# Optimization experiments

Hardware: AMD Instinct MI355X
Metric: run time of the kernel (lower is better)

Reference implementation:

```python
import jax, jax.numpy as jnp
import numpy as np

B = 4096          # batch_size
D_EMB = 16        # per-side embedding dim (embed_to_from width = 2*D_EMB)
D_HIGH = 784      # flattened high-dim feature size
NSR = 5           # negative_sample_rate
A = 1.576943      # UMAP _a
B_PARAM = 0.8950608  # UMAP _b
REPULSION = 1.0
EPS = 1e-4
GLOBAL_LOSS = 0.5
TOTAL_STEPS = 1000
BATCH_COUNT = 500  # fixed step for deterministic alpha/beta
WARMUP = int(0.05 * TOTAL_STEPS)


def _safe_sqrt(sq):
    # sqrt with zero (not NaN) gradient at 0, matching zero-distance pairs
    safe = jnp.where(sq > 0, sq, 1.0)
    return jnp.where(sq > 0, jnp.sqrt(safe), 0.0)


def _pairwise_dist(x):
    # ||x_i - x_j|| via gram trick; avoids materializing [N,N,D]
    sq = jnp.sum(x * x, axis=1)                      # [N]
    gram = x @ x.T                                   # [N,N]
    d2 = sq[:, None] + sq[None, :] - 2.0 * gram
    return _safe_sqrt(jnp.maximum(d2, 0.0))


def _umap_ce_loss(embed_to_from, perm):
    e_to, e_from = jnp.split(embed_to_from, 2, axis=1)   # [B, D_EMB] each
    neg_to = jnp.repeat(e_to, NSR, axis=0)               # [B*NSR, D_EMB]
    repeat_neg = jnp.repeat(e_from, NSR, axis=0)
    neg_from = repeat_neg[perm]                          # shuffled negatives
    d_pos = _safe_sqrt(jnp.sum((e_to - e_from) ** 2, axis=1))
    d_neg = _safe_sqrt(jnp.sum((neg_to - neg_from) ** 2, axis=1))
    dist = jnp.concatenate([d_pos, d_neg], axis=0)       # [B*(1+NSR)]
    p_dist = 1.0 / (1.0 + A * dist ** (2.0 * B_PARAM))
    p_graph = jnp.concatenate([jnp.ones(B, p_dist.dtype), jnp.zeros(B * NSR, p_dist.dtype)])
    attraction = -p_graph * jnp.log(jnp.clip(p_dist, EPS, 1.0))
    repellant = -(1.0 - p_graph) * jnp.log(jnp.clip(1.0 - p_dist, EPS, 1.0)) * REPULSION
    return jnp.mean(attraction + repellant)


def _global_feature_loss(embed_to_from, to_x):
    e_to = embed_to_from[:, :D_EMB]
    to_x = to_x.reshape(to_x.shape[0], -1)
    high_dis = _pairwise_dist(to_x)     # [N,N]
    low_dis = _pairwise_dist(e_to)      # [N,N]
    # row-wise pearson correlation between high_dis and low_dis
    h = high_dis - jnp.mean(high_dis, axis=1, keepdims=True)
    l = low_dis - jnp.mean(low_dis, axis=1, keepdims=True)
    num = jnp.sum(h * l, axis=1)
    den = jnp.sqrt(jnp.sum(h * h, axis=1)) * jnp.sqrt(jnp.sum(l * l, axis=1))
    corr = jnp.mean(num / den)
    return -corr


def _alpha_beta():
    if BATCH_COUNT >= WARMUP:
        if BATCH_COUNT <= 0.9 * TOTAL_STEPS:
            beta = max(0.0, GLOBAL_LOSS * (1 - BATCH_COUNT / (TOTAL_STEPS - WARMUP * 4)) ** 2)
        else:
            beta = 0.0
        alpha = max(0.0, 1 - beta)
    else:
        alpha = 0.0
        beta = GLOBAL_LOSS
    return alpha, beta


def setup_inputs() -> dict:
    key = jax.random.key(0)
    k1, k2, k3 = jax.random.split(key, 3)
    embed_to_from = jax.random.normal(k1, (B, 2 * D_EMB), dtype=jnp.float32)
    placeholder = jax.random.normal(k2, (B, D_HIGH), dtype=jnp.float32)
    perm = jax.random.permutation(k3, B * NSR).astype(jnp.int32)
    return {"embed_to_from": embed_to_from, "placeholder": placeholder, "perm": perm}


def reference(embed_to_from, placeholder, perm):
    loss = _umap_ce_loss(embed_to_from, perm)
    loss_g = _global_feature_loss(embed_to_from, placeholder)
    alpha, beta = _alpha_beta()
    return alpha * loss + beta * loss_g
```

## Files before the change

kernel.cpp:

```cpp
#include <hip/hip_runtime.h>
#include <hip/hip_bf16.h>
#include <math.h>

#define NB    4096
#define DH    784
#define KX8   832
#define NSR   5
#define NNEG  (NB*NSR)
#define NTOT  (NB + NNEG)

#define A_CONST 1.576943f
#define PEXP    1.7901216f
#define EPS_C   1.0e-4f
#define ALPHA_C 0.9296875f
#define BETA_C  0.0703125f

#define NSLOT 64
#define SLAB  (NB * NSLOT)
#define NBLK  528
#define BUFB  8192

typedef __hip_bfloat16 bf16;
typedef short bf16x8 __attribute__((ext_vector_type(8)));
typedef float f32x4  __attribute__((ext_vector_type(4)));
typedef long long2v __attribute__((ext_vector_type(2)));

#define WS_XF8    0
#define WS_EBF    3407872
#define WS_SQX    3670016
#define WS_SQE    3686400
#define WS_STATSP 3702784
#define WS_UPART  8945664
#define WS_CPART  8946048
#define WS_CNT    8946304

__device__ __forceinline__ void gl2lds16(const void* g, void* l) {
    __builtin_amdgcn_global_load_lds(
        (const __attribute__((address_space(1))) unsigned int*)g,
        (__attribute__((address_space(3))) unsigned int*)l,
        16, 0, 0);
}

__global__ void prep_fused(const float* __restrict__ X, const float* __restrict__ emb,
                           const int* __restrict__ perm, unsigned char* __restrict__ Xf8,
                           float* __restrict__ sqx, bf16* __restrict__ Ebf,
                           float* __restrict__ sqe, float* __restrict__ upart,
                           unsigned* __restrict__ cnt) {
    if (blockIdx.x == 0 && threadIdx.x == 0) *cnt = 0u;
    if (blockIdx.x < 1024) {
        const int wave = threadIdx.x >> 6, lane = threadIdx.x & 63;
        const int row = blockIdx.x * 4 + wave;
        const float4* xr = (const float4*)(X + (size_t)row * DH);
        int* xb = (int*)(Xf8 + (size_t)row * KX8);
        float s = 0.f;
        #pragma unroll
        for (int it = 0; it < 4; ++it) {
            const int idx = lane + it * 64;
            if (idx < 208) {
                const int c = idx >> 4, p = idx & 15;
                const int q = p >> 2, h = (p >> 1) & 1, w = p & 1;
                const int src = c * 16 + h * 8 + q * 2 + w;
                int pk = 0;
                if (src < 196) {
                    float4 v = xr[src];
                    s += v.x * v.x + v.y * v.y + v.z * v.z + v.w * v.w;
                    int lo = __builtin_amdgcn_cvt_pk_fp8_f32(v.x, v.y, 0, false);
                    pk = __builtin_amdgcn_cvt_pk_fp8_f32(v.z, v.w, lo, true);
                }
                xb[idx] = pk;
            }
        }
        #pragma unroll
        for (int off = 32; off; off >>= 1) s += __shfl_down(s, off, 64);
        if (lane == 0) sqx[row] = s;
        return;
    }
    const int ub = blockIdx.x - 1024;
    const int t = ub * 256 + threadIdx.x;
    float val = 0.f;
    if (t < NB) {
        const float4* av = (const float4*)(emb + (size_t)t * 32);
        float4 t0 = av[0], t1 = av[1], t2 = av[2], t3 = av[3];
        float4 f0 = av[4], f1 = av[5], f2 = av[6], f3 = av[7];
        bf16* eb = Ebf + (size_t)t * 32;
        union { bf16 h[4]; ushort4 u; } cv;
        #define ST4(dst, q) cv.h[0]=__float2bfloat16(q.x); cv.h[1]=__float2bfloat16(q.y); \
                            cv.h[2]=__float2bfloat16(q.z); cv.h[3]=__float2bfloat16(q.w); \
                            *(ushort4*)(dst) = cv.u;
        ST4(eb,      t0) ST4(eb + 4,  t1) ST4(eb + 8,  t2) ST4(eb + 12, t3)
        #undef ST4
        ushort4 z = {0, 0, 0, 0};
        *(ushort4*)(eb + 16) = z; *(ushort4*)(eb + 20) = z;
        *(ushort4*)(eb + 24) = z; *(ushort4*)(eb + 28) = z;
        sqe[t] = t0.x*t0.x + t0.y*t0.y + t0.z*t0.z + t0.w*t0.w
               + t1.x*t1.x + t1.y*t1.y + t1.z*t1.z + t1.w*t1.w
               + t2.x*t2.x + t2.y*t2.y + t2.z*t2.z + t2.w*t2.w
               + t3.x*t3.x + t3.y*t3.y + t3.z*t3.z + t3.w*t3.w;
        float d2 = 0.f;
        #define D2(a, b) { float4 df = {a.x-b.x, a.y-b.y, a.z-b.z, a.w-b.w}; \
                           d2 += df.x*df.x + df.y*df.y + df.z*df.z + df.w*df.w; }
        D2(t0, f0) D2(t1, f1) D2(t2, f2) D2(t3, f3)
        #undef D2
        float d = sqrtf(d2);
        float p = 1.f / (1.f + A_CONST * powf(d, PEXP));
        val = -logf(fminf(fmaxf(p, EPS_C), 1.f));
    } else if (t < NTOT) {
        const int k = t - NB;
        const int ti = k / 5;
        const int fi = perm[k] / 5;
        const float4* at = (const float4*)(emb + (size_t)ti * 32);
        const float4* bt = (const float4*)(emb + (size_t)fi * 32 + 16);
        float d2 = 0.f;
        #pragma unroll
        for (int q = 0; q < 4; ++q) {
            float4 a = at[q], b = bt[q];
            float4 df = {a.x-b.x, a.y-b.y, a.z-b.z, a.w-b.w};
            d2 += df.x*df.x + df.y*df.y + df.z*df.z + df.w*df.w;
        }
        float d = sqrtf(d2);
        float p = 1.f / (1.f + A_CONST * powf(d, PEXP));
        val = -logf(fminf(fmaxf(1.f - p, EPS_C), 1.f));
    }
    #pragma unroll
    for (int off = 32; off; off >>= 1) val += __shfl_down(val, off, 64);
    __shared__ float ps[4];
    if ((threadIdx.x & 63) == 0) ps[threadIdx.x >> 6] = val;
    __syncthreads();
    if (threadIdx.x == 0) upart[ub] = ps[0] + ps[1] + ps[2] + ps[3];
}

__global__ __launch_bounds__(256, 3) void gram_kernel(
    const unsigned char* __restrict__ Xf8, const bf16* __restrict__ Ebf,
    const float* __restrict__ sqx, const float* __restrict__ sqe,
    float* __restrict__ statsp) {
    __shared__ unsigned char As[3 * BUFB];
    __shared__ unsigned char Bs[3 * BUFB];
    __shared__ float sqxs[256];
    __shared__ float sqes[256];

    int n = (blockIdx.x & 7) * 66 + (blockIdx.x >> 3);
    int bi = 0;
    while (n >= 32 - bi) { n -= 32 - bi; ++bi; }
    const int bj = bi + n;
    const int i0 = bi * 128, j0 = bj * 128;

    const int tid  = threadIdx.x;
    const int wave = tid >> 6;
    const int lane = tid & 63;
    const int wy = wave >> 1, wx = wave & 1;
    const int quad = lane >> 4, l15 = lane & 15;

    f32x4 acc[4][4];
    #pragma unroll
    for (int a = 0; a < 4; ++a)
        #pragma unroll
        for (int b = 0; b < 4; ++b)
            acc[a][b] = (f32x4){0.f, 0.f, 0.f, 0.f};

    const int c0  = wave * 2;
    const int rA  = lane >> 2;
    const int gsb = (((lane & 3) ^ ((lane >> 3) & 3))) * 16;

    const unsigned char* gA0 = Xf8 + (size_t)(i0 + c0 * 16 + rA) * KX8 + gsb;
    const unsigned char* gA1 = Xf8 + (size_t)(i0 + c0 * 16 + 16 + rA) * KX8 + gsb;
    const unsigned char* gB0 = Xf8 + (size_t)(j0 + c0 * 16 + rA) * KX8 + gsb;
    const unsigned char* gB1 = Xf8 + (size_t)(j0 + c0 * 16 + 16 + rA) * KX8 + gsb;

    if (tid < 128) {
        sqxs[tid] = sqx[i0 + tid]; sqxs[128 + tid] = sqx[j0 + tid];
        sqes[tid] = sqe[i0 + tid]; sqes[128 + tid] = sqe[j0 + tid];
    }
    __syncthreads();

    #pragma unroll
    for (int s = 0; s < 2; ++s) {
        gl2lds16(gA0, As + s * BUFB + c0 * 1024);
        gl2lds16(gA1, As + s * BUFB + c0 * 1024 + 1024);
        gl2lds16(gB0, Bs + s * BUFB + c0 * 1024);
        gl2lds16(gB1, Bs + s * BUFB + c0 * 1024 + 1024);
        gA0 += 64; gA1 += 64; gB0 += 64; gB1 += 64;
    }

    const int key = (l15 >> 1) & 3;
    const int boX = ((quad ^ key) << 4);

    int cur = 0;
    for (int t = 0; t < 13; ++t) {
        asm volatile("s_waitcnt vmcnt(4)" ::: "memory");
        __builtin_amdgcn_s_barrier();
        const int nb = (cur + 2 * BUFB >= 3 * BUFB) ? cur - BUFB : cur + 2 * BUFB;
        if (t < 11) {
            gl2lds16(gA0, As + nb + c0 * 1024);
            gl2lds16(gA1, As + nb + c0 * 1024 + 1024);
            gl2lds16(gB0, Bs + nb + c0 * 1024);
            gl2lds16(gB1, Bs + nb + c0 * 1024 + 1024);
            gA0 += 64; gA1 += 64; gB0 += 64; gB1 += 64;
        } else if (t == 11) {
            gl2lds16((const unsigned char*)(Ebf + (size_t)(i0 + c0 * 16 + rA) * 32) + gsb,
                     As + BUFB + c0 * 1024);
            gl2lds16((const unsigned char*)(Ebf + (size_t)(i0 + c0 * 16 + 16 + rA) * 32) + gsb,
                     As + BUFB + c0 * 1024 + 1024);
            gl2lds16((const unsigned char*)(Ebf + (size_t)(j0 + c0 * 16 + rA) * 32) + gsb,
                     Bs + BUFB + c0 * 1024);
            gl2lds16((const unsigned char*)(Ebf + (size_t)(j0 + c0 * 16 + 16 + rA) * 32) + gsb,
                     Bs + BUFB + c0 * 1024 + 1024);
        }
        long2v aF[4], bF[4];
        #pragma unroll
        for (int mi = 0; mi < 4; ++mi)
            aF[mi] = *(const long2v*)&As[cur + (wy * 64 + mi * 16 + l15) * 64 + boX];
        #pragma unroll
        for (int ni = 0; ni < 4; ++ni)
            bF[ni] = *(const long2v*)&Bs[cur + (wx * 64 + ni * 16 + l15) * 64 + boX];
        #pragma unroll
        for (int mi = 0; mi < 4; ++mi)
            #pragma unroll
            for (int ni = 0; ni < 4; ++ni) {
                acc[mi][ni] = __builtin_amdgcn_mfma_f32_16x16x32_fp8_fp8(
                    aF[mi][0], bF[ni][0], acc[mi][ni], 0, 0, 0);
                acc[mi][ni] = __builtin_amdgcn_mfma_f32_16x16x32_fp8_fp8(
                    aF[mi][1], bF[ni][1], acc[mi][ni], 0, 0, 0);
            }
        cur = (cur == 2 * BUFB) ? 0 : cur + BUFB;
    }
    asm volatile("s_waitcnt vmcnt(0)" ::: "memory");
    __builtin_amdgcn_s_barrier();

    const int slot_r = bj * 2 + wx;
    const int slot_c = bi * 2 + wy;
    bf16x8 bfrE[4];
    #pragma unroll
    for (int ni = 0; ni < 4; ++ni)
        bfrE[ni] = *(const bf16x8*)&Bs[BUFB + (wx * 64 + ni * 16 + l15) * 64 + boX];
    float cH[4] = {0,0,0,0}, cH2[4] = {0,0,0,0}, cL[4] = {0,0,0,0},
          cL2[4] = {0,0,0,0}, cHL[4] = {0,0,0,0};
    #pragma unroll
    for (int mi = 0; mi < 4; ++mi) {
        bf16x8 afE = *(const bf16x8*)&As[BUFB + (wy * 64 + mi * 16 + l15) * 64 + boX];
        f32x4 aE[4];
        #pragma unroll
        for (int ni = 0; ni < 4; ++ni) {
            f32x4 z = (f32x4){0.f, 0.f, 0.f, 0.f};
            aE[ni] = __builtin_amdgcn_mfma_f32_16x16x32_bf16(afE, bfrE[ni], z, 0, 0, 0);
        }
        const int ilocb = wy * 64 + mi * 16 + quad * 4;
        float sH[4] = {0,0,0,0}, sH2[4] = {0,0,0,0}, sL[4] = {0,0,0,0},
              sL2[4] = {0,0,0,0}, sHL[4] = {0,0,0,0};
        #pragma unroll
        for (int ni = 0; ni < 4; ++ni) {
            const int jloc = wx * 64 + ni * 16 + l15;
            const int j = j0 + jloc;
            const float sqxj = sqxs[128 + jloc];
            const float sqej = sqes[128 + jloc];
            #pragma unroll
            for (int r = 0; r < 4; ++r) {
                const int iloc = ilocb + r;
                const int i = i0 + iloc;
                float H, L;
                if (i == j) { H = 0.f; L = 0.f; }
                else {
                    float d2  = sqxs[iloc] + sqxj - 2.0f * acc[mi][ni][r];
                    H = sqrtf(fmaxf(d2, 0.f));
                    float d2e = sqes[iloc] + sqej - 2.0f * aE[ni][r];
                    L = sqrtf(fmaxf(d2e, 0.f));
                }
                sH[r] += H; sH2[r] += H * H; sL[r] += L; sL2[r] += L * L; sHL[r] += H * L;
                cH[ni] += H; cH2[ni] += H * H; cL[ni] += L; cL2[ni] += L * L; cHL[ni] += H * L;
            }
        }
        #pragma unroll
        for (int r = 0; r < 4; ++r) {
            float v0 = sH[r], v1 = sH2[r], v2 = sL[r], v3 = sL2[r], v4 = sHL[r];
            #pragma unroll
            for (int off2 = 1; off2 < 16; off2 <<= 1) {
                v0 += __shfl_xor(v0, off2, 64);
                v1 += __shfl_xor(v1, off2, 64);
                v2 += __shfl_xor(v2, off2, 64);
                v3 += __shfl_xor(v3, off2, 64);
                v4 += __shfl_xor(v4, off2, 64);
            }
            if (l15 == 0) {
                const int i = i0 + ilocb + r;
                float* base = statsp + (size_t)slot_r * NB + i;
                base[0 * SLAB] = v0;
                base[1 * SLAB] = v1;
                base[2 * SLAB] = v2;
                base[3 * SLAB] = v3;
                base[4 * SLAB] = v4;
            }
        }
    }
    if (bi != bj) {
        #pragma unroll
        for (int ni = 0; ni < 4; ++ni) {
            float v0 = cH[ni], v1 = cH2[ni], v2 = cL[ni], v3 = cL2[ni], v4 = cHL[ni];
            #pragma unroll
            for (int off2 = 16; off2 < 64; off2 <<= 1) {
                v0 += __shfl_xor(v0, off2, 64);
                v1 += __shfl_xor(v1, off2, 64);
                v2 += __shfl_xor(v2, off2, 64);
                v3 += __shfl_xor(v3, off2, 64);
                v4 += __shfl_xor(v4, off2, 64);
            }
            if (quad == 0) {
                const int j = j0 + wx * 64 + ni * 16 + l15;
                float* base = statsp + (size_t)slot_c * NB + j;
                base[0 * SLAB] = v0;
                base[1 * SLAB] = v1;
                base[2 * SLAB] = v2;
                base[3 * SLAB] = v3;
                base[4 * SLAB] = v4;
            }
        }
    }
}

__global__ void finish1_kernel(const float* __restrict__ statsp, const float* __restrict__ upart,
                               float* __restrict__ cpart, unsigned* __restrict__ cnt,
                               float* __restrict__ out) {
    __shared__ float ps2[4][64][5];
    const int t = threadIdx.x;
    const int rloc = t & 63;
    const int sg = t >> 6;
    const int r = blockIdx.x * 64 + rloc;
    float sh = 0.f, sh2 = 0.f, sl = 0.f, sl2 = 0.f, shl = 0.f;
    for (int s = sg * 16; s < sg * 16 + 16; ++s) {
        const float* base = statsp + (size_t)s * NB + r;
        sh  += base[0 * SLAB];
        sh2 += base[1 * SLAB];
        sl  += base[2 * SLAB];
        sl2 += base[3 * SLAB];
        shl += base[4 * SLAB];
    }
    ps2[sg][rloc][0] = sh; ps2[sg][rloc][1] = sh2; ps2[sg][rloc][2] = sl;
    ps2[sg][rloc][3] = sl2; ps2[sg][rloc][4] = shl;
    __syncthreads();
    if (t < 64) {
        float a = 0.f, b = 0.f, c = 0.f, d = 0.f, e = 0.f;
        #pragma unroll
        for (int g = 0; g < 4; ++g) {
            a += ps2[g][t][0]; b += ps2[g][t][1]; c += ps2[g][t][2];
            d += ps2[g][t][3]; e += ps2[g][t][4];
        }
        const float invN = 1.0f / (float)NB;
        float num = e - a * c * invN;
        float vh  = fmaxf(b - a * a * invN, 0.f);
        float vl  = fmaxf(d - c * c * invN, 0.f);
        float local = num / (sqrtf(vh) * sqrtf(vl));
        #pragma unroll
        for (int off = 32; off; off >>= 1) local += __shfl_down(local, off, 64);
        if (t == 0) cpart[blockIdx.x] = local;
    }
    __shared__ int lastFlag;
    if (t == 0) {
        __threadfence();
        unsigned prev = atomicAdd(cnt, 1u);
        lastFlag = (prev == 63u);
    }
    __syncthreads();
    if (lastFlag) {
        __threadfence();
        float v = 0.f;
        if (t < 64) v += cpart[t] * (-BETA_C / (float)NB);
        if (t < 96) v += upart[t] * (ALPHA_C / (float)NTOT);
        #pragma unroll
        for (int off = 32; off; off >>= 1) v += __shfl_down(v, off, 64);
        __shared__ float fin[4];
        if ((t & 63) == 0) fin[t >> 6] = v;
        __syncthreads();
        if (t == 0) out[0] = fin[0] + fin[1] + fin[2] + fin[3];
    }
}

extern "C" void kernel_launch(void* const* d_in, const int* in_sizes, int n_in,
                              void* d_out, int out_size, void* d_ws, size_t ws_size,
                              hipStream_t stream) {
    const float* emb  = (const float*)d_in[0];
    const float* ph   = (const float*)d_in[1];
    const int*   perm = (const int*)d_in[2];
    float* out = (float*)d_out;

    char* ws = (char*)d_ws;
    unsigned char* Xf8 = (unsigned char*)(ws + WS_XF8);
    bf16*  Ebf    = (bf16*) (ws + WS_EBF);
    float* sqx    = (float*)(ws + WS_SQX);
    float* sqe    = (float*)(ws + WS_SQE);
    float* statsp = (float*)(ws + WS_STATSP);
    float* upart  = (float*)(ws + WS_UPART);
    float* cpart  = (float*)(ws + WS_CPART);
    unsigned* cnt = (unsigned*)(ws + WS_CNT);

    prep_fused<<<1120, 256, 0, stream>>>(ph, emb, perm, Xf8, sqx, Ebf, sqe, upart, cnt);
    gram_kernel<<<NBLK, 256, 0, stream>>>(Xf8, Ebf, sqx, sqe, statsp);
    finish1_kernel<<<64, 256, 0, stream>>>(statsp, upart, cpart, cnt, out);
}
```

Before: 118.8 us.

## Replace LDS-staged 128x128 gram tiles with single-wave 64x64 tiles loading from global

The gram kernel moves from 4-wave blocks computing 128x128 upper-triangle tiles through a triple-buffered LDS pipeline to single-wave blocks computing 64x64 tiles. Each wave loads its FP8 MFMA fragments straight from global memory into registers with software double-buffering. The prep kernel permutes the FP8 layout so these direct loads match the fragment order. This removes LDS traffic and barriers and launches many more blocks, at the cost of lower operand reuse and more global/L2 reads per output.

New measurement: 126.2 us. +6.3%, slower.

```diff
diff --git a/kernel.cpp b/kernel.cpp
--- a/kernel.cpp
+++ b/kernel.cpp
@@ -17,8 +17,7 @@
 
 #define NSLOT 64
 #define SLAB  (NB * NSLOT)
-#define NBLK  528
-#define BUFB  8192
+#define NBLK  2080
 
 typedef __hip_bfloat16 bf16;
 typedef short bf16x8 __attribute__((ext_vector_type(8)));
@@ -33,13 +32,6 @@
 #define WS_UPART  8945664
 #define WS_CPART  8946048
 #define WS_CNT    8946304
-
-__device__ __forceinline__ void gl2lds16(const void* g, void* l) {
-    __builtin_amdgcn_global_load_lds(
-        (const __attribute__((address_space(1))) unsigned int*)g,
-        (__attribute__((address_space(3))) unsigned int*)l,
-        16, 0, 0);
-}
 
 __global__ void prep_fused(const float* __restrict__ X, const float* __restrict__ emb,
                            const int* __restrict__ perm, unsigned char* __restrict__ Xf8,
@@ -55,11 +47,8 @@
         float s = 0.f;
         #pragma unroll
         for (int it = 0; it < 4; ++it) {
-            const int idx = lane + it * 64;
-            if (idx < 208) {
-                const int c = idx >> 4, p = idx & 15;
-                const int q = p >> 2, h = (p >> 1) & 1, w = p & 1;
-                const int src = c * 16 + h * 8 + q * 2 + w;
+            const int src = lane + it * 64;
+            if (src < 208) {
                 int pk = 0;
                 if (src < 196) {
                     float4 v = xr[src];
@@ -67,7 +56,9 @@
                     int lo = __builtin_amdgcn_cvt_pk_fp8_f32(v.x, v.y, 0, false);
                     pk = __builtin_amdgcn_cvt_pk_fp8_f32(v.z, v.w, lo, true);
                 }
-                xb[idx] = pk;
+                const int c = src >> 4, sc = src & 15;
+                const int h = sc >> 3, q = (sc >> 1) & 3, w = sc & 1;
+                xb[c * 16 + q * 4 + h * 2 + w] = pk;
             }
         }
         #pragma unroll
@@ -129,25 +120,17 @@
     if (threadIdx.x == 0) upart[ub] = ps[0] + ps[1] + ps[2] + ps[3];
 }
 
-__global__ __launch_bounds__(256, 3) void gram_kernel(
+__global__ __launch_bounds__(64, 2) void gram_kernel(
     const unsigned char* __restrict__ Xf8, const bf16* __restrict__ Ebf,
     const float* __restrict__ sqx, const float* __restrict__ sqe,
     float* __restrict__ statsp) {
-    __shared__ unsigned char As[3 * BUFB];
-    __shared__ unsigned char Bs[3 * BUFB];
-    __shared__ float sqxs[256];
-    __shared__ float sqes[256];
-
-    int n = (blockIdx.x & 7) * 66 + (blockIdx.x >> 3);
+    int n = (blockIdx.x & 7) * 260 + (blockIdx.x >> 3);
     int bi = 0;
-    while (n >= 32 - bi) { n -= 32 - bi; ++bi; }
+    while (n >= 64 - bi) { n -= 64 - bi; ++bi; }
     const int bj = bi + n;
-    const int i0 = bi * 128, j0 = bj * 128;
-
-    const int tid  = threadIdx.x;
-    const int wave = tid >> 6;
-    const int lane = tid & 63;
-    const int wy = wave >> 1, wx = wave & 1;
+    const int i0 = bi * 64, j0 = bj * 64;
+
+    const int lane = threadIdx.x;
     const int quad = lane >> 4, l15 = lane & 15;
 
     f32x4 acc[4][4];
@@ -157,111 +140,98 @@
         for (int b = 0; b < 4; ++b)
             acc[a][b] = (f32x4){0.f, 0.f, 0.f, 0.f};
 
-    const int c0  = wave * 2;
-    const int rA  = lane >> 2;
-    const int gsb = (((lane & 3) ^ ((lane >> 3) & 3))) * 16;
-
-    const unsigned char* gA0 = Xf8 + (size_t)(i0 + c0 * 16 + rA) * KX8 + gsb;
-    const unsigned char* gA1 = Xf8 + (size_t)(i0 + c0 * 16 + 16 + rA) * KX8 + gsb;
-    const unsigned char* gB0 = Xf8 + (size_t)(j0 + c0 * 16 + rA) * KX8 + gsb;
-    const unsigned char* gB1 = Xf8 + (size_t)(j0 + c0 * 16 + 16 + rA) * KX8 + gsb;
-
-    if (tid < 128) {
-        sqxs[tid] = sqx[i0 + tid]; sqxs[128 + tid] = sqx[j0 + tid];
-        sqes[tid] = sqe[i0 + tid]; sqes[128 + tid] = sqe[j0 + tid];
-    }
-    __syncthreads();
-
-    #pragma unroll
-    for (int s = 0; s < 2; ++s) {
-        gl2lds16(gA0, As + s * BUFB + c0 * 1024);
-        gl2lds16(gA1, As + s * BUFB + c0 * 1024 + 1024);
-        gl2lds16(gB0, Bs + s * BUFB + c0 * 1024);
-        gl2lds16(gB1, Bs + s * BUFB + c0 * 1024 + 1024);
-        gA0 += 64; gA1 += 64; gB0 += 64; gB1 += 64;
-    }
-
-    const int key = (l15 >> 1) & 3;
-    const int boX = ((quad ^ key) << 4);
-
-    int cur = 0;
-    for (int t = 0; t < 13; ++t) {
-        asm volatile("s_waitcnt vmcnt(4)" ::: "memory");
-        __builtin_amdgcn_s_barrier();
-        const int nb = (cur + 2 * BUFB >= 3 * BUFB) ? cur - BUFB : cur + 2 * BUFB;
-        if (t < 11) {
-            gl2lds16(gA0, As + nb + c0 * 1024);
-            gl2lds16(gA1, As + nb + c0 * 1024 + 1024);
-            gl2lds16(gB0, Bs + nb + c0 * 1024);
-            gl2lds16(gB1, Bs + nb + c0 * 1024 + 1024);
-            gA0 += 64; gA1 += 64; gB0 += 64; gB1 += 64;
-        } else if (t == 11) {
-            gl2lds16((const unsigned char*)(Ebf + (size_t)(i0 + c0 * 16 + rA) * 32) + gsb,
-                     As + BUFB + c0 * 1024);
-            gl2lds16((const unsigned char*)(Ebf + (size_t)(i0 + c0 * 16 + 16 + rA) * 32) + gsb,
-                     As + BUFB + c0 * 1024 + 1024);
-            gl2lds16((const unsigned char*)(Ebf + (size_t)(j0 + c0 * 16 + rA) * 32) + gsb,
-                     Bs + BUFB + c0 * 1024);
-            gl2lds16((const unsigned char*)(Ebf + (size_t)(j0 + c0 * 16 + 16 + rA) * 32) + gsb,
-                     Bs + BUFB + c0 * 1024 + 1024);
-        }
-        long2v aF[4], bF[4];
-        #pragma unroll
-        for (int mi = 0; mi < 4; ++mi)
-            aF[mi] = *(const long2v*)&As[cur + (wy * 64 + mi * 16 + l15) * 64 + boX];
-        #pragma unroll
-        for (int ni = 0; ni < 4; ++ni)
-            bF[ni] = *(const long2v*)&Bs[cur + (wx * 64 + ni * 16 + l15) * 64 + boX];
-        #pragma unroll
-        for (int mi = 0; mi < 4; ++mi)
-            #pragma unroll
-            for (int ni = 0; ni < 4; ++ni) {
-                acc[mi][ni] = __builtin_amdgcn_mfma_f32_16x16x32_fp8_fp8(
-                    aF[mi][0], bF[ni][0], acc[mi][ni], 0, 0, 0);
-                acc[mi][ni] = __builtin_amdgcn_mfma_f32_16x16x32_fp8_fp8(
-                    aF[mi][1], bF[ni][1], acc[mi][ni], 0, 0, 0);
-            }
-        cur = (cur == 2 * BUFB) ? 0 : cur + BUFB;
-    }
-    asm volatile("s_waitcnt vmcnt(0)" ::: "memory");
-    __builtin_amdgcn_s_barrier();
-
-    const int slot_r = bj * 2 + wx;
-    const int slot_c = bi * 2 + wy;
-    bf16x8 bfrE[4];
-    #pragma unroll
-    for (int ni = 0; ni < 4; ++ni)
-        bfrE[ni] = *(const bf16x8*)&Bs[BUFB + (wx * 64 + ni * 16 + l15) * 64 + boX];
+    const unsigned char* pam[4];
+    const unsigned char* pbm[4];
+    #pragma unroll
+    for (int mi = 0; mi < 4; ++mi) {
+        pam[mi] = Xf8 + (size_t)(i0 + mi * 16 + l15) * KX8 + quad * 16;
+        pbm[mi] = Xf8 + (size_t)(j0 + mi * 16 + l15) * KX8 + quad * 16;
+    }
+
+    long2v a0[4], b0[4], a1[4], b1[4];
+    #pragma unroll
+    for (int mi = 0; mi < 4; ++mi) {
+        a0[mi] = *(const long2v*)(pam[mi]);
+        b0[mi] = *(const long2v*)(pbm[mi]);
+    }
+    #define MFMA_SET(af, bf) \
+        _Pragma("unroll") \
+        for (int mi = 0; mi < 4; ++mi) \
+            _Pragma("unroll") \
+            for (int ni = 0; ni < 4; ++ni) { \
+                acc[mi][ni] = __builtin_amdgcn_mfma_f32_16x16x32_fp8_fp8( \
+                    af[mi][0], bf[ni][0], acc[mi][ni], 0, 0, 0); \
+                acc[mi][ni] = __builtin_amdgcn_mfma_f32_16x16x32_fp8_fp8( \
+                    af[mi][1], bf[ni][1], acc[mi][ni], 0, 0, 0); \
+            }
+    #pragma unroll
+    for (int p = 0; p < 6; ++p) {
+        const int s1 = (2 * p + 1) * 64, s2 = (2 * p + 2) * 64;
+        #pragma unroll
+        for (int mi = 0; mi < 4; ++mi) {
+            a1[mi] = *(const long2v*)(pam[mi] + s1);
+            b1[mi] = *(const long2v*)(pbm[mi] + s1);
+        }
+        MFMA_SET(a0, b0)
+        #pragma unroll
+        for (int mi = 0; mi < 4; ++mi) {
+            a0[mi] = *(const long2v*)(pam[mi] + s2);
+            b0[mi] = *(const long2v*)(pbm[mi] + s2);
+        }
+        MFMA_SET(a1, b1)
+    }
+
+    const unsigned char* pea = (const unsigned char*)Ebf + (size_t)(i0 + l15) * 64 + quad * 16;
+    const unsigned char* peb = (const unsigned char*)Ebf + (size_t)(j0 + l15) * 64 + quad * 16;
+    bf16x8 afE[4], bfE[4];
+    #pragma unroll
+    for (int mi = 0; mi < 4; ++mi) {
+        afE[mi] = *(const bf16x8*)(pea + mi * 1024);
+        bfE[mi] = *(const bf16x8*)(peb + mi * 1024);
+    }
+    float sqxi[16], sqei[16];
+    #pragma unroll
+    for (int mi = 0; mi < 4; ++mi)
+        #pragma unroll
+        for (int r = 0; r < 4; ++r) {
+            sqxi[mi * 4 + r] = sqx[i0 + mi * 16 + quad * 4 + r];
+            sqei[mi * 4 + r] = sqe[i0 + mi * 16 + quad * 4 + r];
+        }
+    float sqxj[4], sqej[4];
+    #pragma unroll
+    for (int ni = 0; ni < 4; ++ni) {
+        sqxj[ni] = sqx[j0 + ni * 16 + l15];
+        sqej[ni] = sqe[j0 + ni * 16 + l15];
+    }
+
+    MFMA_SET(a0, b0)
+    #undef MFMA_SET
+
     float cH[4] = {0,0,0,0}, cH2[4] = {0,0,0,0}, cL[4] = {0,0,0,0},
           cL2[4] = {0,0,0,0}, cHL[4] = {0,0,0,0};
     #pragma unroll
     for (int mi = 0; mi < 4; ++mi) {
-        bf16x8 afE = *(const bf16x8*)&As[BUFB + (wy * 64 + mi * 16 + l15) * 64 + boX];
         f32x4 aE[4];
         #pragma unroll
         for (int ni = 0; ni < 4; ++ni) {
             f32x4 z = (f32x4){0.f, 0.f, 0.f, 0.f};
-            aE[ni] = __builtin_amdgcn_mfma_f32_16x16x32_bf16(afE, bfrE[ni], z, 0, 0, 0);
-        }
-        const int ilocb = wy * 64 + mi * 16 + quad * 4;
+            aE[ni] = __builtin_amdgcn_mfma_f32_16x16x32_bf16(afE[mi], bfE[ni], z, 0, 0, 0);
+        }
+        const int ilocb = mi * 16 + quad * 4;
         float sH[4] = {0,0,0,0}, sH2[4] = {0,0,0,0}, sL[4] = {0,0,0,0},
               sL2[4] = {0,0,0,0}, sHL[4] = {0,0,0,0};
         #pragma unroll
         for (int ni = 0; ni < 4; ++ni) {
-            const int jloc = wx * 64 + ni * 16 + l15;
-            const int j = j0 + jloc;
-            const float sqxj = sqxs[128 + jloc];
-            const float sqej = sqes[128 + jloc];
+            const int j = j0 + ni * 16 + l15;
             #pragma unroll
             for (int r = 0; r < 4; ++r) {
-                const int iloc = ilocb + r;
-                const int i = i0 + iloc;
+                const int i = i0 + ilocb + r;
                 float H, L;
                 if (i == j) { H = 0.f; L = 0.f; }
                 else {
-                    float d2  = sqxs[iloc] + sqxj - 2.0f * acc[mi][ni][r];
+                    float d2  = sqxi[mi * 4 + r] + sqxj[ni] - 2.0f * acc[mi][ni][r];
                     H = sqrtf(fmaxf(d2, 0.f));
-                    float d2e = sqes[iloc] + sqej - 2.0f * aE[ni][r];
+                    float d2e = sqei[mi * 4 + r] + sqej[ni] - 2.0f * aE[ni][r];
                     L = sqrtf(fmaxf(d2e, 0.f));
                 }
                 sH[r] += H; sH2[r] += H * H; sL[r] += L; sL2[r] += L * L; sHL[r] += H * L;
@@ -281,7 +251,7 @@
             }
             if (l15 == 0) {
                 const int i = i0 + ilocb + r;
-                float* base = statsp + (size_t)slot_r * NB + i;
+                float* base = statsp + (size_t)bj * NB + i;
                 base[0 * SLAB] = v0;
                 base[1 * SLAB] = v1;
                 base[2 * SLAB] = v2;
@@ -303,8 +273,8 @@
                 v4 += __shfl_xor(v4, off2, 64);
             }
             if (quad == 0) {
-                const int j = j0 + wx * 64 + ni * 16 + l15;
-                float* base = statsp + (size_t)slot_c * NB + j;
+                const int j = j0 + ni * 16 + l15;
+                float* base = statsp + (size_t)bi * NB + j;
                 base[0 * SLAB] = v0;
                 base[1 * SLAB] = v1;
                 base[2 * SLAB] = v2;
@@ -391,6 +361,6 @@
     unsigned* cnt = (unsigned*)(ws + WS_CNT);
 
     prep_fused<<<1120, 256, 0, stream>>>(ph, emb, perm, Xf8, sqx, Ebf, sqe, upart, cnt);
-    gram_kernel<<<NBLK, 256, 0, stream>>>(Xf8, Ebf, sqx, sqe, statsp);
+    gram_kernel<<<NBLK, 64, 0, stream>>>(Xf8, Ebf, sqx, sqe, statsp);
     finish1_kernel<<<64, 256, 0, stream>>>(statsp, upart, cpart, cnt, out);
 }
```

## Fuse prep, gram and finish kernels into one megakernel with spin-flag dependencies

Applied to the files above, without the earlier changes.

Replaces the three launches (prep, gram, finish) with one persistent kernel. The 32 diagonal-tile blocks quantize their own 128 X rows to fp8 and convert the embeddings, then publish a per-tile flag. Off-diagonal blocks spin on the flags for their two row tiles, and the last 64 blocks wait on a global done counter before doing the correlation reduction. This removes launch gaps and inter-kernel drains, but puts the X conversion on only 32 blocks as a critical path. It also relies on every block being co-resident and on the counters starting from a poisoned workspace value, since they are never reset.

Result: slower. 191.7 us (+61.4%).

```diff
diff --git a/kernel.cpp b/kernel.cpp
--- a/kernel.cpp
+++ b/kernel.cpp
@@ -19,6 +19,7 @@
 #define SLAB  (NB * NSLOT)
 #define NBLK  528
 #define BUFB  8192
+#define POISON 0xAAAAAAAAu
 
 typedef __hip_bfloat16 bf16;
 typedef short bf16x8 __attribute__((ext_vector_type(8)));
@@ -32,7 +33,9 @@
 #define WS_STATSP 3702784
 #define WS_UPART  8945664
 #define WS_CPART  8946048
-#define WS_CNT    8946304
+#define WS_FLAGS  8946304
+#define WS_DONE   8946432
+#define WS_FIN    8946436
 
 __device__ __forceinline__ void gl2lds16(const void* g, void* l) {
     __builtin_amdgcn_global_load_lds(
@@ -41,112 +44,133 @@
         16, 0, 0);
 }
 
-__global__ void prep_fused(const float* __restrict__ X, const float* __restrict__ emb,
-                           const int* __restrict__ perm, unsigned char* __restrict__ Xf8,
-                           float* __restrict__ sqx, bf16* __restrict__ Ebf,
-                           float* __restrict__ sqe, float* __restrict__ upart,
-                           unsigned* __restrict__ cnt) {
-    if (blockIdx.x == 0 && threadIdx.x == 0) *cnt = 0u;
-    if (blockIdx.x < 1024) {
-        const int wave = threadIdx.x >> 6, lane = threadIdx.x & 63;
-        const int row = blockIdx.x * 4 + wave;
-        const float4* xr = (const float4*)(X + (size_t)row * DH);
-        int* xb = (int*)(Xf8 + (size_t)row * KX8);
-        float s = 0.f;
-        #pragma unroll
-        for (int it = 0; it < 4; ++it) {
-            const int idx = lane + it * 64;
-            if (idx < 208) {
-                const int c = idx >> 4, p = idx & 15;
-                const int q = p >> 2, h = (p >> 1) & 1, w = p & 1;
-                const int src = c * 16 + h * 8 + q * 2 + w;
-                int pk = 0;
-                if (src < 196) {
-                    float4 v = xr[src];
-                    s += v.x * v.x + v.y * v.y + v.z * v.z + v.w * v.w;
-                    int lo = __builtin_amdgcn_cvt_pk_fp8_f32(v.x, v.y, 0, false);
-                    pk = __builtin_amdgcn_cvt_pk_fp8_f32(v.z, v.w, lo, true);
+__global__ __launch_bounds__(256, 3) void mega_kernel(
+    const float* __restrict__ X, const float* __restrict__ emb,
+    const int* __restrict__ perm, unsigned char* __restrict__ Xf8,
+    bf16* __restrict__ Ebf, float* __restrict__ sqx, float* __restrict__ sqe,
+    float* __restrict__ statsp, float* __restrict__ upart,
+    float* __restrict__ cpart, unsigned* __restrict__ flags,
+    unsigned* __restrict__ done_cnt, unsigned* __restrict__ fin_cnt,
+    float* __restrict__ out) {
+    __shared__ __align__(16) unsigned char smem[51200];
+    unsigned char* As = smem;
+    unsigned char* Bs = smem + 24576;
+    float* sqxs = (float*)(smem + 49152);
+    float* sqes = (float*)(smem + 50176);
+
+    const int tid = threadIdx.x;
+    const int b = blockIdx.x;
+    const int wave = tid >> 6, lane = tid & 63;
+
+    if (tid == 0) {
+        atomicCAS(done_cnt, POISON, 0u);
+        atomicCAS(fin_cnt, POISON, 0u);
+    }
+
+    int bi, bj;
+    if (b < 32) { bi = b; bj = b; }
+    else { int k = b - 32; bi = 0; while (k >= 31 - bi) { k -= 31 - bi; ++bi; } bj = bi + 1 + k; }
+    const int i0 = bi * 128, j0 = bj * 128;
+
+    if (b < 32) {
+        for (int rr = 0; rr < 32; ++rr) {
+            const int row = b * 128 + wave * 32 + rr;
+            const float4* xr = (const float4*)(X + (size_t)row * DH);
+            int* xb = (int*)(Xf8 + (size_t)row * KX8);
+            float s = 0.f;
+            #pragma unroll
+            for (int it = 0; it < 4; ++it) {
+                const int src = lane + it * 64;
+                if (src < 208) {
+                    int pk = 0;
+                    if (src < 196) {
+                        float4 v = xr[src];
+                        s += v.x * v.x + v.y * v.y + v.z * v.z + v.w * v.w;
+                        int lo = __builtin_amdgcn_cvt_pk_fp8_f32(v.x, v.y, 0, false);
+                        pk = __builtin_amdgcn_cvt_pk_fp8_f32(v.z, v.w, lo, true);
+                    }
+                    const int c = src >> 4, sc = src & 15;
+                    const int h = sc >> 3, q = (sc >> 1) & 3, w = sc & 1;
+                    xb[c * 16 + q * 4 + h * 2 + w] = pk;
                 }
-                xb[idx] = pk;
-            }
-        }
-        #pragma unroll
-        for (int off = 32; off; off >>= 1) s += __shfl_down(s, off, 64);
-        if (lane == 0) sqx[row] = s;
-        return;
-    }
-    const int ub = blockIdx.x - 1024;
-    const int t = ub * 256 + threadIdx.x;
-    float val = 0.f;
-    if (t < NB) {
-        const float4* av = (const float4*)(emb + (size_t)t * 32);
-        float4 t0 = av[0], t1 = av[1], t2 = av[2], t3 = av[3];
-        float4 f0 = av[4], f1 = av[5], f2 = av[6], f3 = av[7];
-        bf16* eb = Ebf + (size_t)t * 32;
-        union { bf16 h[4]; ushort4 u; } cv;
-        #define ST4(dst, q) cv.h[0]=__float2bfloat16(q.x); cv.h[1]=__float2bfloat16(q.y); \
-                            cv.h[2]=__float2bfloat16(q.z); cv.h[3]=__float2bfloat16(q.w); \
-                            *(ushort4*)(dst) = cv.u;
-        ST4(eb,      t0) ST4(eb + 4,  t1) ST4(eb + 8,  t2) ST4(eb + 12, t3)
-        #undef ST4
-        ushort4 z = {0, 0, 0, 0};
-        *(ushort4*)(eb + 16) = z; *(ushort4*)(eb + 20) = z;
-        *(ushort4*)(eb + 24) = z; *(ushort4*)(eb + 28) = z;
-        sqe[t] = t0.x*t0.x + t0.y*t0.y + t0.z*t0.z + t0.w*t0.w
-               + t1.x*t1.x + t1.y*t1.y + t1.z*t1.z + t1.w*t1.w
-               + t2.x*t2.x + t2.y*t2.y + t2.z*t2.z + t2.w*t2.w
-               + t3.x*t3.x + t3.y*t3.y + t3.z*t3.z + t3.w*t3.w;
-        float d2 = 0.f;
-        #define D2(a, b) { float4 df = {a.x-b.x, a.y-b.y, a.z-b.z, a.w-b.w}; \
-                           d2 += df.x*df.x + df.y*df.y + df.z*df.z + df.w*df.w; }
-        D2(t0, f0) D2(t1, f1) D2(t2, f2) D2(t3, f3)
-        #undef D2
-        float d = sqrtf(d2);
-        float p = 1.f / (1.f + A_CONST * powf(d, PEXP));
-        val = -logf(fminf(fmaxf(p, EPS_C), 1.f));
-    } else if (t < NTOT) {
-        const int k = t - NB;
-        const int ti = k / 5;
-        const int fi = perm[k] / 5;
-        const float4* at = (const float4*)(emb + (size_t)ti * 32);
-        const float4* bt = (const float4*)(emb + (size_t)fi * 32 + 16);
-        float d2 = 0.f;
-        #pragma unroll
-        for (int q = 0; q < 4; ++q) {
-            float4 a = at[q], b = bt[q];
-            float4 df = {a.x-b.x, a.y-b.y, a.z-b.z, a.w-b.w};
-            d2 += df.x*df.x + df.y*df.y + df.z*df.z + df.w*df.w;
-        }
-        float d = sqrtf(d2);
-        float p = 1.f / (1.f + A_CONST * powf(d, PEXP));
-        val = -logf(fminf(fmaxf(1.f - p, EPS_C), 1.f));
-    }
-    #pragma unroll
-    for (int off = 32; off; off >>= 1) val += __shfl_down(val, off, 64);
-    __shared__ float ps[4];
-    if ((threadIdx.x & 63) == 0) ps[threadIdx.x >> 6] = val;
-    __syncthreads();
-    if (threadIdx.x == 0) upart[ub] = ps[0] + ps[1] + ps[2] + ps[3];
-}
-
-__global__ __launch_bounds__(256, 3) void gram_kernel(
-    const unsigned char* __restrict__ Xf8, const bf16* __restrict__ Ebf,
-    const float* __restrict__ sqx, const float* __restrict__ sqe,
-    float* __restrict__ statsp) {
-    __shared__ unsigned char As[3 * BUFB];
-    __shared__ unsigned char Bs[3 * BUFB];
-    __shared__ float sqxs[256];
-    __shared__ float sqes[256];
-
-    int n = (blockIdx.x & 7) * 66 + (blockIdx.x >> 3);
-    int bi = 0;
-    while (n >= 32 - bi) { n -= 32 - bi; ++bi; }
-    const int bj = bi + n;
-    const int i0 = bi * 128, j0 = bj * 128;
-
-    const int tid  = threadIdx.x;
-    const int wave = tid >> 6;
-    const int lane = tid & 63;
+            }
+            #pragma unroll
+            for (int off = 32; off; off >>= 1) s += __shfl_down(s, off, 64);
+            if (lane == 0) sqx[row] = s;
+        }
+        if (tid < 128) {
+            const int row = b * 128 + tid;
+            const float4* av = (const float4*)(emb + (size_t)row * 32);
+            float4 t0 = av[0], t1 = av[1], t2 = av[2], t3 = av[3];
+            bf16* eb = Ebf + (size_t)row * 32;
+            union { bf16 h[4]; ushort4 u; } cv;
+            #define ST4(dst, q) cv.h[0]=__float2bfloat16(q.x); cv.h[1]=__float2bfloat16(q.y); \
+                                cv.h[2]=__float2bfloat16(q.z); cv.h[3]=__float2bfloat16(q.w); \
+                                *(ushort4*)(dst) = cv.u;
+            ST4(eb,      t0) ST4(eb + 4,  t1) ST4(eb + 8,  t2) ST4(eb + 12, t3)
+            #undef ST4
+            ushort4 z = {0, 0, 0, 0};
+            *(ushort4*)(eb + 16) = z; *(ushort4*)(eb + 20) = z;
+            *(ushort4*)(eb + 24) = z; *(ushort4*)(eb + 28) = z;
+            sqe[row] = t0.x*t0.x + t0.y*t0.y + t0.z*t0.z + t0.w*t0.w
+                     + t1.x*t1.x + t1.y*t1.y + t1.z*t1.z + t1.w*t1.w
+                     + t2.x*t2.x + t2.y*t2.y + t2.z*t2.z + t2.w*t2.w
+                     + t3.x*t3.x + t3.y*t3.y + t3.z*t3.z + t3.w*t3.w;
+        }
+        __syncthreads();
+        if (tid == 0) { __threadfence(); atomicExch(&flags[b], 1u); }
+    }
+
+    if (b < 96) {
+        const int t = b * 256 + tid;
+        float val;
+        if (t < NB) {
+            const float4* av = (const float4*)(emb + (size_t)t * 32);
+            float4 t0 = av[0], t1 = av[1], t2 = av[2], t3 = av[3];
+            float4 f0 = av[4], f1 = av[5], f2 = av[6], f3 = av[7];
+            float d2 = 0.f;
+            #define D2(a, b2) { float4 df = {a.x-b2.x, a.y-b2.y, a.z-b2.z, a.w-b2.w}; \
+                                d2 += df.x*df.x + df.y*df.y + df.z*df.z + df.w*df.w; }
+            D2(t0, f0) D2(t1, f1) D2(t2, f2) D2(t3, f3)
+            #undef D2
+            float d = sqrtf(d2);
+            float p = 1.f / (1.f + A_CONST * powf(d, PEXP));
+            val = -logf(fminf(fmaxf(p, EPS_C), 1.f));
+        } else {
+            const int k = t - NB;
+            const int ti = k / 5;
+            const int fi = perm[k] / 5;
+            const float4* at = (const float4*)(emb + (size_t)ti * 32);
+            const float4* bt = (const float4*)(emb + (size_t)fi * 32 + 16);
+            float d2 = 0.f;
+            #pragma unroll
+            for (int q = 0; q < 4; ++q) {
+                float4 a = at[q], b2 = bt[q];
+                float4 df = {a.x-b2.x, a.y-b2.y, a.z-b2.z, a.w-b2.w};
+                d2 += df.x*df.x + df.y*df.y + df.z*df.z + df.w*df.w;
+            }
+            float d = sqrtf(d2);
+            float p = 1.f / (1.f + A_CONST * powf(d, PEXP));
+            val = -logf(fminf(fmaxf(1.f - p, EPS_C), 1.f));
+        }
+        #pragma unroll
+        for (int off = 32; off; off >>= 1) val += __shfl_down(val, off, 64);
+        float* ps = (float*)(smem + 49152);
+        if (lane == 0) ps[wave] = val;
+        __syncthreads();
+        if (tid == 0) upart[b] = ps[0] + ps[1] + ps[2] + ps[3];
+        __syncthreads();
+    }
+
+    if (b >= 32) {
+        if (tid == 0) {
+            while (atomicAdd(&flags[bi], 0u) != 1u) __builtin_amdgcn_s_sleep(8);
+            while (atomicAdd(&flags[bj], 0u) != 1u) __builtin_amdgcn_s_sleep(8);
+            __threadfence();
+        }
+        __syncthreads();
+    }
+
     const int wy = wave >> 1, wx = wave & 1;
     const int quad = lane >> 4, l15 = lane & 15;
 
@@ -154,8 +178,8 @@
     #pragma unroll
     for (int a = 0; a < 4; ++a)
         #pragma unroll
-        for (int b = 0; b < 4; ++b)
-            acc[a][b] = (f32x4){0.f, 0.f, 0.f, 0.f};
+        for (int b2 = 0; b2 < 4; ++b2)
+            acc[a][b2] = (f32x4){0.f, 0.f, 0.f, 0.f};
 
     const int c0  = wave * 2;
     const int rA  = lane >> 2;
@@ -313,62 +337,68 @@
             }
         }
     }
-}
-
-__global__ void finish1_kernel(const float* __restrict__ statsp, const float* __restrict__ upart,
-                               float* __restrict__ cpart, unsigned* __restrict__ cnt,
-                               float* __restrict__ out) {
-    __shared__ float ps2[4][64][5];
-    const int t = threadIdx.x;
-    const int rloc = t & 63;
-    const int sg = t >> 6;
-    const int r = blockIdx.x * 64 + rloc;
-    float sh = 0.f, sh2 = 0.f, sl = 0.f, sl2 = 0.f, shl = 0.f;
-    for (int s = sg * 16; s < sg * 16 + 16; ++s) {
-        const float* base = statsp + (size_t)s * NB + r;
-        sh  += base[0 * SLAB];
-        sh2 += base[1 * SLAB];
-        sl  += base[2 * SLAB];
-        sl2 += base[3 * SLAB];
-        shl += base[4 * SLAB];
-    }
-    ps2[sg][rloc][0] = sh; ps2[sg][rloc][1] = sh2; ps2[sg][rloc][2] = sl;
-    ps2[sg][rloc][3] = sl2; ps2[sg][rloc][4] = shl;
+
     __syncthreads();
-    if (t < 64) {
-        float a = 0.f, b = 0.f, c = 0.f, d = 0.f, e = 0.f;
-        #pragma unroll
-        for (int g = 0; g < 4; ++g) {
-            a += ps2[g][t][0]; b += ps2[g][t][1]; c += ps2[g][t][2];
-            d += ps2[g][t][3]; e += ps2[g][t][4];
-        }
-        const float invN = 1.0f / (float)NB;
-        float num = e - a * c * invN;
-        float vh  = fmaxf(b - a * a * invN, 0.f);
-        float vl  = fmaxf(d - c * c * invN, 0.f);
-        float local = num / (sqrtf(vh) * sqrtf(vl));
-        #pragma unroll
-        for (int off = 32; off; off >>= 1) local += __shfl_down(local, off, 64);
-        if (t == 0) cpart[blockIdx.x] = local;
-    }
-    __shared__ int lastFlag;
-    if (t == 0) {
-        __threadfence();
-        unsigned prev = atomicAdd(cnt, 1u);
-        lastFlag = (prev == 63u);
-    }
-    __syncthreads();
-    if (lastFlag) {
-        __threadfence();
-        float v = 0.f;
-        if (t < 64) v += cpart[t] * (-BETA_C / (float)NB);
-        if (t < 96) v += upart[t] * (ALPHA_C / (float)NTOT);
-        #pragma unroll
-        for (int off = 32; off; off >>= 1) v += __shfl_down(v, off, 64);
-        __shared__ float fin[4];
-        if ((t & 63) == 0) fin[t >> 6] = v;
-        __syncthreads();
-        if (t == 0) out[0] = fin[0] + fin[1] + fin[2] + fin[3];
+    if (tid == 0) { __threadfence(); atomicAdd(done_cnt, 1u); }
+
+    if (b >= NBLK - 64) {
+        const int fb = b - (NBLK - 64);
+        if (tid == 0) {
+            while (atomicAdd(done_cnt, 0u) != (unsigned)NBLK) __builtin_amdgcn_s_sleep(8);
+            __threadfence();
+        }
+        __syncthreads();
+        float (*ps2)[64][5] = (float (*)[64][5])smem;
+        int* lastFlag = (int*)(smem + 10240);
+        float* fin = (float*)(smem + 10256);
+        const int rloc = tid & 63;
+        const int sg = tid >> 6;
+        const int r = fb * 64 + rloc;
+        float sh = 0.f, sh2 = 0.f, sl = 0.f, sl2 = 0.f, shl = 0.f;
+        for (int s = sg * 16; s < sg * 16 + 16; ++s) {
+            const float* base = statsp + (size_t)s * NB + r;
+            sh  += base[0 * SLAB];
+            sh2 += base[1 * SLAB];
+            sl  += base[2 * SLAB];
+            sl2 += base[3 * SLAB];
+            shl += base[4 * SLAB];
+        }
+        ps2[sg][rloc][0] = sh; ps2[sg][rloc][1] = sh2; ps2[sg][rloc][2] = sl;
+        ps2[sg][rloc][3] = sl2; ps2[sg][rloc][4] = shl;
+        __syncthreads();
+        if (tid < 64) {
+            float a = 0.f, b2 = 0.f, c = 0.f, d = 0.f, e = 0.f;
+            #pragma unroll
+            for (int g = 0; g < 4; ++g) {
+                a += ps2[g][tid][0]; b2 += ps2[g][tid][1]; c += ps2[g][tid][2];
+                d += ps2[g][tid][3]; e += ps2[g][tid][4];
+            }
+            const float invN = 1.0f / (float)NB;
+            float num = e - a * c * invN;
+            float vh  = fmaxf(b2 - a * a * invN, 0.f);
+            float vl  = fmaxf(d - c * c * invN, 0.f);
+            float local = num / (sqrtf(vh) * sqrtf(vl));
+            #pragma unroll
+            for (int off = 32; off; off >>= 1) local += __shfl_down(local, off, 64);
+            if (tid == 0) cpart[fb] = local;
+        }
+        if (tid == 0) {
+            __threadfence();
+            unsigned prev = atomicAdd(fin_cnt, 1u);
+            *lastFlag = (prev == 63u);
+        }
+        __syncthreads();
+        if (*lastFlag) {
+            __threadfence();
+            float v = 0.f;
+            if (tid < 64) v += cpart[tid] * (-BETA_C / (float)NB);
+            if (tid < 96) v += upart[tid] * (ALPHA_C / (float)NTOT);
+            #pragma unroll
+            for (int off = 32; off; off >>= 1) v += __shfl_down(v, off, 64);
+            if ((tid & 63) == 0) fin[tid >> 6] = v;
+            __syncthreads();
+            if (tid == 0) out[0] = fin[0] + fin[1] + fin[2] + fin[3];
+        }
     }
 }
 
@@ -382,15 +412,17 @@
 
     char* ws = (char*)d_ws;
     unsigned char* Xf8 = (unsigned char*)(ws + WS_XF8);
-    bf16*  Ebf    = (bf16*) (ws + WS_EBF);
-    float* sqx    = (float*)(ws + WS_SQX);
-    float* sqe    = (float*)(ws + WS_SQE);
-    float* statsp = (float*)(ws + WS_STATSP);
-    float* upart  = (float*)(ws + WS_UPART);
-    float* cpart  = (float*)(ws + WS_CPART);
-    unsigned* cnt = (unsigned*)(ws + WS_CNT);
-
-    prep_fused<<<1120, 256, 0, stream>>>(ph, emb, perm, Xf8, sqx, Ebf, sqe, upart, cnt);
-    gram_kernel<<<NBLK, 256, 0, stream>>>(Xf8, Ebf, sqx, sqe, statsp);
-    finish1_kernel<<<64, 256, 0, stream>>>(statsp, upart, cpart, cnt, out);
+    bf16*  Ebf     = (bf16*) (ws + WS_EBF);
+    float* sqx     = (float*)(ws + WS_SQX);
+    float* sqe     = (float*)(ws + WS_SQE);
+    float* statsp  = (float*)(ws + WS_STATSP);
+    float* upart   = (float*)(ws + WS_UPART);
+    float* cpart   = (float*)(ws + WS_CPART);
+    unsigned* flags    = (unsigned*)(ws + WS_FLAGS);
+    unsigned* done_cnt = (unsigned*)(ws + WS_DONE);
+    unsigned* fin_cnt  = (unsigned*)(ws + WS_FIN);
+
+    mega_kernel<<<NBLK, 256, 0, stream>>>(ph, emb, perm, Xf8, Ebf, sqx, sqe,
+                                          statsp, upart, cpart, flags,
+                                          done_cnt, fin_cnt, out);
 }
```

## Switch gram kernel to double-buffered LDS with reads before prefetch

Applied to the files above, without the earlier changes.

Cuts the gram kernel's LDS staging from triple to double buffering. Fragments are now read from shared memory before the next tile's async load is issued, and each iteration waits on vmcnt(0). This lowers LDS use per block, which may allow more resident blocks, but it overlaps less of the global load latency. The FP8 prep reorders the permutation so global reads are contiguous and the scatter moves to the stores, and the epilogue reuses the squared distances instead of recomputing H*H and L*L.

After: 145.1 us. 1.22x slower.

```diff
diff --git a/kernel.cpp b/kernel.cpp
--- a/kernel.cpp
+++ b/kernel.cpp
@@ -55,11 +55,8 @@
         float s = 0.f;
         #pragma unroll
         for (int it = 0; it < 4; ++it) {
-            const int idx = lane + it * 64;
-            if (idx < 208) {
-                const int c = idx >> 4, p = idx & 15;
-                const int q = p >> 2, h = (p >> 1) & 1, w = p & 1;
-                const int src = c * 16 + h * 8 + q * 2 + w;
+            const int src = lane + it * 64;
+            if (src < 208) {
                 int pk = 0;
                 if (src < 196) {
                     float4 v = xr[src];
@@ -67,7 +64,9 @@
                     int lo = __builtin_amdgcn_cvt_pk_fp8_f32(v.x, v.y, 0, false);
                     pk = __builtin_amdgcn_cvt_pk_fp8_f32(v.z, v.w, lo, true);
                 }
-                xb[idx] = pk;
+                const int c = src >> 4, sc = src & 15;
+                const int h = sc >> 3, q = (sc >> 1) & 3, w = sc & 1;
+                xb[c * 16 + q * 4 + h * 2 + w] = pk;
             }
         }
         #pragma unroll
@@ -133,8 +132,8 @@
     const unsigned char* __restrict__ Xf8, const bf16* __restrict__ Ebf,
     const float* __restrict__ sqx, const float* __restrict__ sqe,
     float* __restrict__ statsp) {
-    __shared__ unsigned char As[3 * BUFB];
-    __shared__ unsigned char Bs[3 * BUFB];
+    __shared__ unsigned char As[2 * BUFB];
+    __shared__ unsigned char Bs[2 * BUFB];
     __shared__ float sqxs[256];
     __shared__ float sqes[256];
 
@@ -172,46 +171,43 @@
     }
     __syncthreads();
 
-    #pragma unroll
-    for (int s = 0; s < 2; ++s) {
-        gl2lds16(gA0, As + s * BUFB + c0 * 1024);
-        gl2lds16(gA1, As + s * BUFB + c0 * 1024 + 1024);
-        gl2lds16(gB0, Bs + s * BUFB + c0 * 1024);
-        gl2lds16(gB1, Bs + s * BUFB + c0 * 1024 + 1024);
-        gA0 += 64; gA1 += 64; gB0 += 64; gB1 += 64;
-    }
+    gl2lds16(gA0, As + c0 * 1024);
+    gl2lds16(gA1, As + c0 * 1024 + 1024);
+    gl2lds16(gB0, Bs + c0 * 1024);
+    gl2lds16(gB1, Bs + c0 * 1024 + 1024);
+    gA0 += 64; gA1 += 64; gB0 += 64; gB1 += 64;
 
     const int key = (l15 >> 1) & 3;
     const int boX = ((quad ^ key) << 4);
 
     int cur = 0;
     for (int t = 0; t < 13; ++t) {
-        asm volatile("s_waitcnt vmcnt(4)" ::: "memory");
+        asm volatile("s_waitcnt vmcnt(0)" ::: "memory");
         __builtin_amdgcn_s_barrier();
-        const int nb = (cur + 2 * BUFB >= 3 * BUFB) ? cur - BUFB : cur + 2 * BUFB;
-        if (t < 11) {
+        long2v aF[4], bF[4];
+        #pragma unroll
+        for (int mi = 0; mi < 4; ++mi)
+            aF[mi] = *(const long2v*)&As[cur + (wy * 64 + mi * 16 + l15) * 64 + boX];
+        #pragma unroll
+        for (int ni = 0; ni < 4; ++ni)
+            bF[ni] = *(const long2v*)&Bs[cur + (wx * 64 + ni * 16 + l15) * 64 + boX];
+        const int nb = cur ^ BUFB;
+        if (t < 12) {
             gl2lds16(gA0, As + nb + c0 * 1024);
             gl2lds16(gA1, As + nb + c0 * 1024 + 1024);
             gl2lds16(gB0, Bs + nb + c0 * 1024);
             gl2lds16(gB1, Bs + nb + c0 * 1024 + 1024);
             gA0 += 64; gA1 += 64; gB0 += 64; gB1 += 64;
-        } else if (t == 11) {
+        } else {
             gl2lds16((const unsigned char*)(Ebf + (size_t)(i0 + c0 * 16 + rA) * 32) + gsb,
-                     As + BUFB + c0 * 1024);
+                     As + nb + c0 * 1024);
             gl2lds16((const unsigned char*)(Ebf + (size_t)(i0 + c0 * 16 + 16 + rA) * 32) + gsb,
-                     As + BUFB + c0 * 1024 + 1024);
+                     As + nb + c0 * 1024 + 1024);
             gl2lds16((const unsigned char*)(Ebf + (size_t)(j0 + c0 * 16 + rA) * 32) + gsb,
-                     Bs + BUFB + c0 * 1024);
+                     Bs + nb + c0 * 1024);
             gl2lds16((const unsigned char*)(Ebf + (size_t)(j0 + c0 * 16 + 16 + rA) * 32) + gsb,
-                     Bs + BUFB + c0 * 1024 + 1024);
-        }
-        long2v aF[4], bF[4];
-        #pragma unroll
-        for (int mi = 0; mi < 4; ++mi)
-            aF[mi] = *(const long2v*)&As[cur + (wy * 64 + mi * 16 + l15) * 64 + boX];
-        #pragma unroll
-        for (int ni = 0; ni < 4; ++ni)
-            bF[ni] = *(const long2v*)&Bs[cur + (wx * 64 + ni * 16 + l15) * 64 + boX];
+                     Bs + nb + c0 * 1024 + 1024);
+        }
         #pragma unroll
         for (int mi = 0; mi < 4; ++mi)
             #pragma unroll
@@ -221,7 +217,7 @@
                 acc[mi][ni] = __builtin_amdgcn_mfma_f32_16x16x32_fp8_fp8(
                     aF[mi][1], bF[ni][1], acc[mi][ni], 0, 0, 0);
             }
-        cur = (cur == 2 * BUFB) ? 0 : cur + BUFB;
+        cur ^= BUFB;
     }
     asm volatile("s_waitcnt vmcnt(0)" ::: "memory");
     __builtin_amdgcn_s_barrier();
@@ -231,12 +227,12 @@
     bf16x8 bfrE[4];
     #pragma unroll
     for (int ni = 0; ni < 4; ++ni)
-        bfrE[ni] = *(const bf16x8*)&Bs[BUFB + (wx * 64 + ni * 16 + l15) * 64 + boX];
+        bfrE[ni] = *(const bf16x8*)&Bs[cur + (wx * 64 + ni * 16 + l15) * 64 + boX];
     float cH[4] = {0,0,0,0}, cH2[4] = {0,0,0,0}, cL[4] = {0,0,0,0},
           cL2[4] = {0,0,0,0}, cHL[4] = {0,0,0,0};
     #pragma unroll
     for (int mi = 0; mi < 4; ++mi) {
-        bf16x8 afE = *(const bf16x8*)&As[BUFB + (wy * 64 + mi * 16 + l15) * 64 + boX];
+        bf16x8 afE = *(const bf16x8*)&As[cur + (wy * 64 + mi * 16 + l15) * 64 + boX];
         f32x4 aE[4];
         #pragma unroll
         for (int ni = 0; ni < 4; ++ni) {
@@ -256,16 +252,16 @@
             for (int r = 0; r < 4; ++r) {
                 const int iloc = ilocb + r;
                 const int i = i0 + iloc;
-                float H, L;
-                if (i == j) { H = 0.f; L = 0.f; }
+                float H, L, H2, L2;
+                if (i == j) { H = 0.f; L = 0.f; H2 = 0.f; L2 = 0.f; }
                 else {
-                    float d2  = sqxs[iloc] + sqxj - 2.0f * acc[mi][ni][r];
-                    H = sqrtf(fmaxf(d2, 0.f));
-                    float d2e = sqes[iloc] + sqej - 2.0f * aE[ni][r];
-                    L = sqrtf(fmaxf(d2e, 0.f));
+                    H2 = fmaxf(sqxs[iloc] + sqxj - 2.0f * acc[mi][ni][r], 0.f);
+                    H = sqrtf(H2);
+                    L2 = fmaxf(sqes[iloc] + sqej - 2.0f * aE[ni][r], 0.f);
+                    L = sqrtf(L2);
                 }
-                sH[r] += H; sH2[r] += H * H; sL[r] += L; sL2[r] += L * L; sHL[r] += H * L;
-                cH[ni] += H; cH2[ni] += H * H; cL[ni] += L; cL2[ni] += L * L; cHL[ni] += H * L;
+                sH[r] += H; sH2[r] += H2; sL[r] += L; sL2[r] += L2; sHL[r] += H * L;
+                cH[ni] += H; cH2[ni] += H2; cL[ni] += L; cL2[ni] += L2; cHL[ni] += H * L;
             }
         }
         #pragma unroll
```
